# Optimization experiments

Measured on AMD Instinct MI355X. Metric: run time of the kernel, lower is better.

The kernel has to match this reference:

```python
import jax, jax.numpy as jnp
import numpy as np

N_TX = 50000; N_ADDR = 50000; E = 500000
IN = 128; C = 128; H = 4; D = 32  # C = hidden_channels = H*D
G = 512; OUT = 2
NEG_SLOPE = 0.2  # PyG HANConv default negative_slope


def _gat(h_src, h_dst, src, dst, a_src, a_dst, n_dst):
    # h_*: [N, H, D]; a_*: [H, D]; src/dst: [E]
    al_s = jnp.sum(h_src * a_src, axis=-1)  # [N_src, H]
    al_d = jnp.sum(h_dst * a_dst, axis=-1)  # [N_dst, H]
    alpha = jax.nn.leaky_relu(al_s[src] + al_d[dst], NEG_SLOPE)  # [E, H]
    # softmax over incoming edges of each destination node
    amax = jax.ops.segment_max(alpha, dst, num_segments=n_dst)
    ex = jnp.exp(alpha - amax[dst])
    denom = jax.ops.segment_sum(ex, dst, num_segments=n_dst)
    w = ex / (denom[dst] + 1e-16)  # PyG softmax adds 1e-16
    out = jax.ops.segment_sum(h_src[src] * w[:, :, None], dst, num_segments=n_dst)
    return jax.nn.relu(out.reshape(n_dst, H * D))


def _semantic(xs, q, Wk, bk):
    out = jnp.stack(xs)  # [K, N, C]
    score = jnp.sum(q * jnp.tanh(out @ Wk + bk).mean(axis=1), axis=-1)  # [K]
    attn = jax.nn.softmax(score)
    return jnp.sum(attn[:, None, None] * out, axis=0)  # [N, C]


def setup_inputs() -> dict:
    key = jax.random.key(0)
    k = jax.random.split(key, 24)
    s = 0.05
    return {
        "x_tx": jax.random.normal(k[0], (N_TX, IN), jnp.float32),
        "x_addr": jax.random.normal(k[1], (N_ADDR, IN), jnp.float32),
        "ei_ta": jnp.stack([jax.random.randint(k[2], (E,), 0, N_TX),
                            jax.random.randint(k[3], (E,), 0, N_ADDR)]),
        "ei_at": jnp.stack([jax.random.randint(k[4], (E,), 0, N_ADDR),
                            jax.random.randint(k[5], (E,), 0, N_TX)]),
        "ei_tt": jnp.stack([jax.random.randint(k[6], (E,), 0, N_TX),
                            jax.random.randint(k[7], (E,), 0, N_TX)]),
        "batch_tx": jnp.sort(jax.random.randint(k[8], (N_TX,), 0, G)),
        "W_tx": jax.random.normal(k[9], (IN, C), jnp.float32) / np.sqrt(IN).astype(np.float32),
        "b_tx": jnp.zeros((C,), jnp.float32),
        "W_addr": jax.random.normal(k[10], (IN, C), jnp.float32) / np.sqrt(IN).astype(np.float32),
        "b_addr": jnp.zeros((C,), jnp.float32),
        "a_src_ta": jax.random.normal(k[11], (H, D), jnp.float32) * s,
        "a_dst_ta": jax.random.normal(k[12], (H, D), jnp.float32) * s,
        "a_src_at": jax.random.normal(k[13], (H, D), jnp.float32) * s,
        "a_dst_at": jax.random.normal(k[14], (H, D), jnp.float32) * s,
        "a_src_tt": jax.random.normal(k[15], (H, D), jnp.float32) * s,
        "a_dst_tt": jax.random.normal(k[16], (H, D), jnp.float32) * s,
        "Wk": jax.random.normal(k[17], (C, C), jnp.float32) / np.sqrt(C).astype(np.float32),
        "bk": jnp.zeros((C,), jnp.float32),
        "q": jax.random.normal(k[18], (C,), jnp.float32) * s,
        "Wl": jax.random.normal(k[19], (C, OUT), jnp.float32) / np.sqrt(C).astype(np.float32),
        "bl": jnp.zeros((OUT,), jnp.float32),
    }


def reference(x_tx, x_addr, ei_ta, ei_at, ei_tt, batch_tx,
              W_tx, b_tx, W_addr, b_addr,
              a_src_ta, a_dst_ta, a_src_at, a_dst_at, a_src_tt, a_dst_tt,
              Wk, bk, q, Wl, bl):
    # per-node-type projection
    h_tx = (x_tx @ W_tx + b_tx).reshape(N_TX, H, D)
    h_ad = (x_addr @ W_addr + b_addr).reshape(N_ADDR, H, D)
    # per-edge-type GAT message passing (dropout disabled: eval mode)
    out_ta = _gat(h_tx, h_ad, ei_ta[0], ei_ta[1], a_src_ta, a_dst_ta, N_ADDR)
    out_at = _gat(h_ad, h_tx, ei_at[0], ei_at[1], a_src_at, a_dst_at, N_TX)
    out_tt = _gat(h_tx, h_tx, ei_tt[0], ei_tt[1], a_src_tt, a_dst_tt, N_TX)
    # semantic attention across metapaths ending at 'transaction'
    tx_feat = _semantic([out_at, out_tt], q, Wk, bk)  # [N_TX, C]
    # global_mean_pool over graph assignment
    sums = jax.ops.segment_sum(tx_feat, batch_tx, num_segments=G)
    cnts = jax.ops.segment_sum(jnp.ones((N_TX,), tx_feat.dtype), batch_tx, num_segments=G)
    pooled = sums / jnp.maximum(cnts, 1.0)[:, None]  # [G, C]
    return pooled @ Wl + bl  # [G, OUT]
```

## Files before the change

### kernel.cpp

```cpp
#include <hip/hip_runtime.h>

#define NTX   50000
#define NADDR 50000
#define NE    500000
#define GG    512
#define NEG   0.2f
#define MBLK  64
#define PBM   782
#define NCHUNK 196
#define GBLK  3125

typedef _Float16 f16;
typedef f16 f16x4 __attribute__((ext_vector_type(4)));
typedef f16 f16x8 __attribute__((ext_vector_type(8)));
typedef float f32x2 __attribute__((ext_vector_type(2)));
typedef float f32x4 __attribute__((ext_vector_type(4)));

__device__ __forceinline__ float lrelu(float x) { return x > 0.f ? x : NEG * x; }

__global__ __launch_bounds__(256) void prep_kernel(
    const float* __restrict__ W_tx, const float* __restrict__ W_ad,
    const float* __restrict__ Wk,
    f16* __restrict__ Wt_tx, f16* __restrict__ Wt_ad, f16* __restrict__ Wkt)
{
    const float* W = (blockIdx.y == 0) ? W_tx : (blockIdx.y == 1) ? W_ad : Wk;
    f16* Wt        = (blockIdx.y == 0) ? Wt_tx : (blockIdx.y == 1) ? Wt_ad : Wkt;
    __shared__ f16 tile[32][136];
    const int t = threadIdx.x;
    const int j0 = blockIdx.x * 32;
    for (int i = t; i < 32 * 128; i += 256) {
        int r = i >> 7, c = i & 127;
        tile[r][c] = (f16)W[(size_t)(j0 + r) * 128 + c];
    }
    __syncthreads();
    for (int i = t; i < 128 * 8; i += 256) {
        int c = i >> 3, q = i & 7;
        f16x4 p = { tile[q * 4 + 0][c], tile[q * 4 + 1][c],
                    tile[q * 4 + 2][c], tile[q * 4 + 3][c] };
        *(f16x4*)&Wt[(size_t)c * 128 + j0 + q * 4] = p;
    }
}

__global__ __launch_bounds__(256) void proj2_kernel(
    const float* __restrict__ x_tx, const f16* __restrict__ Wt_txg,
    const float* __restrict__ b_tx, f16* __restrict__ h_tx,
    const float* __restrict__ x_ad, const f16* __restrict__ Wt_adg,
    const float* __restrict__ b_ad, f16* __restrict__ h_ad,
    const float* __restrict__ a_dat, float* __restrict__ al_dat,
    const float* __restrict__ a_stt, float* __restrict__ al_stt,
    const float* __restrict__ a_dtt, float* __restrict__ al_dtt,
    const float* __restrict__ a_sat, float* __restrict__ al_sat)
{
    __shared__ f16 Wt[128][136];
    __shared__ f16 xt[MBLK][136];
    const bool is_tx = blockIdx.x < PBM;
    const float* x  = is_tx ? x_tx : x_ad;
    const f16* Wtg  = is_tx ? Wt_txg : Wt_adg;
    const float* b  = is_tx ? b_tx : b_ad;
    f16* h          = is_tx ? h_tx : h_ad;
    const int row0 = (is_tx ? blockIdx.x : blockIdx.x - PBM) * MBLK;
    const int t = threadIdx.x;

    {
        const f16x8* G = (const f16x8*)Wtg;
        for (int i = t; i < 128 * 16; i += 256) {
            int r = i >> 4, q = i & 15;
            *(f16x8*)&Wt[r][q * 8] = G[i];
        }
    }
    for (int i = t; i < MBLK * 32; i += 256) {
        int r = i >> 5, q = i & 31;
        int gr = row0 + r; if (gr >= NTX) gr = NTX - 1;
        float4 v = ((const float4*)x)[(size_t)gr * 32 + q];
        f16x4 p = {(f16)v.x, (f16)v.y, (f16)v.z, (f16)v.w};
        *(f16x4*)&xt[r][q * 4] = p;
    }
    __syncthreads();

    const int l = t & 63, w = t >> 6;
    const int l15 = l & 15, lq = l >> 4;

    f16x8 afrag[4];
#pragma unroll
    for (int kt = 0; kt < 4; kt++)
        afrag[kt] = *(const f16x8*)&xt[w * 16 + l15][kt * 32 + lq * 8];

    f32x4 acc[8];
#pragma unroll
    for (int n = 0; n < 8; n++) {
        float bc = b[n * 16 + l15];
        acc[n] = (f32x4){bc, bc, bc, bc};
#pragma unroll
        for (int kt = 0; kt < 4; kt++) {
            f16x8 bfrag = *(const f16x8*)&Wt[n * 16 + l15][kt * 32 + lq * 8];
            acc[n] = __builtin_amdgcn_mfma_f32_16x16x32_f16(afrag[kt], bfrag, acc[n], 0, 0, 0);
        }
    }

#pragma unroll
    for (int r = 0; r < 4; r++) {
        int row = row0 + w * 16 + lq * 4 + r;
        if (row < NTX) {
#pragma unroll
            for (int n = 0; n < 8; n++)
                h[(size_t)row * 128 + n * 16 + l15] = (f16)acc[n][r];
        }
    }

    auto do_dot = [&](const float* __restrict__ a, float* __restrict__ al) {
        float av[8];
#pragma unroll
        for (int n = 0; n < 8; n++) av[n] = a[n * 16 + l15];
#pragma unroll
        for (int r = 0; r < 4; r++) {
            float p0 = acc[0][r] * av[0] + acc[1][r] * av[1];
            float p1 = acc[2][r] * av[2] + acc[3][r] * av[3];
            float p2 = acc[4][r] * av[4] + acc[5][r] * av[5];
            float p3 = acc[6][r] * av[6] + acc[7][r] * av[7];
#pragma unroll
            for (int o = 1; o < 16; o <<= 1) {
                p0 += __shfl_xor(p0, o); p1 += __shfl_xor(p1, o);
                p2 += __shfl_xor(p2, o); p3 += __shfl_xor(p3, o);
            }
            int row = row0 + w * 16 + lq * 4 + r;
            if (l15 == 0 && row < NTX) {
                float4 v = make_float4(p0, p1, p2, p3);
                *(float4*)&al[(size_t)row * 4] = v;
            }
        }
    };
    if (is_tx) { do_dot(a_dat, al_dat); do_dot(a_stt, al_stt); do_dot(a_dtt, al_dtt); }
    else       { do_dot(a_sat, al_sat); }
}

__global__ __launch_bounds__(256) void deg2_kernel(
    const int* __restrict__ ei0, const int* __restrict__ ei1,
    int* __restrict__ deg0, int* __restrict__ deg1,
    int* __restrict__ rank0, int* __restrict__ rank1)
{
    int idx = blockIdx.x * 256 + threadIdx.x;
    if (idx < NE) rank0[idx] = atomicAdd(&deg0[ei0[NE + idx]], 1);
    else if (idx < 2 * NE) rank1[idx - NE] = atomicAdd(&deg1[ei1[NE + (idx - NE)]], 1);
}

__global__ __launch_bounds__(256) void chunksum_kernel(
    const int* __restrict__ deg0, const int* __restrict__ deg1,
    int* __restrict__ csum)
{
    const int* deg = blockIdx.y == 0 ? deg0 : deg1;
    __shared__ int s[256];
    const int t = threadIdx.x;
    int idx = blockIdx.x * 256 + t;
    s[t] = idx < NTX ? deg[idx] : 0;
    __syncthreads();
    for (int o = 128; o > 0; o >>= 1) {
        if (t < o) s[t] += s[t + o];
        __syncthreads();
    }
    if (t == 0) csum[blockIdx.y * NCHUNK + blockIdx.x] = s[0];
}

__global__ __launch_bounds__(256) void chunkscan_kernel(int* __restrict__ csum)
{
    __shared__ int s[256];
    const int t = threadIdx.x;
    int* base = csum + blockIdx.x * NCHUNK;
    int v = t < NCHUNK ? base[t] : 0;
    s[t] = v;
    __syncthreads();
    for (int o = 1; o < 256; o <<= 1) {
        int u = (t >= o) ? s[t - o] : 0;
        __syncthreads();
        s[t] += u;
        __syncthreads();
    }
    if (t < NCHUNK) base[t] = s[t] - v;
}

__global__ __launch_bounds__(256) void scanwrite_kernel(
    const int* __restrict__ deg0, const int* __restrict__ deg1,
    const int* __restrict__ csum,
    int* __restrict__ row0, int* __restrict__ row1)
{
    const int* deg = blockIdx.y == 0 ? deg0 : deg1;
    int* row       = blockIdx.y == 0 ? row0 : row1;
    __shared__ int s[256];
    const int t = threadIdx.x;
    int idx = blockIdx.x * 256 + t;
    int v = idx < NTX ? deg[idx] : 0;
    s[t] = v;
    __syncthreads();
    for (int o = 1; o < 256; o <<= 1) {
        int u = (t >= o) ? s[t - o] : 0;
        __syncthreads();
        s[t] += u;
        __syncthreads();
    }
    if (idx < NTX)
        row[idx] = s[t] - v + csum[blockIdx.y * NCHUNK + blockIdx.x];
}

__global__ __launch_bounds__(256) void fill2_kernel(
    const int* __restrict__ ei0, const int* __restrict__ rank0,
    const int* __restrict__ row0, int* __restrict__ csr0,
    const int* __restrict__ ei1, const int* __restrict__ rank1,
    const int* __restrict__ row1, int* __restrict__ csr1)
{
    int idx = blockIdx.x * 256 + threadIdx.x;
    const int* ei; const int* rank; const int* row; int* csr;
    int e;
    if (idx < NE)          { ei = ei0; rank = rank0; row = row0; csr = csr0; e = idx; }
    else if (idx < 2 * NE) { ei = ei1; rank = rank1; row = row1; csr = csr1; e = idx - NE; }
    else return;
    int s = ei[e];
    int d = ei[NE + e];
    csr[row[d] + rank[e]] = s;
}

__global__ __launch_bounds__(256) void gat_gather2_kernel(
    const int* __restrict__ row_at, const int* __restrict__ deg_at,
    const int* __restrict__ csr_at, const float* __restrict__ als_at,
    const float* __restrict__ ald_at, const f16* __restrict__ h_at,
    f16* __restrict__ out_at,
    const int* __restrict__ row_tt, const int* __restrict__ deg_tt,
    const int* __restrict__ csr_tt, const float* __restrict__ als_tt,
    const float* __restrict__ ald_tt, const f16* __restrict__ h_tt,
    f16* __restrict__ out_tt)
{
    const int bid = blockIdx.x;
    const bool at = ((bid & 4) == 0);
    const int dblk = (bid >> 3) * 4 + (bid & 3);
    if (dblk >= GBLK) return;

    const int* rs = at ? row_at : row_tt;
    const int* dg = at ? deg_at : deg_tt;
    const int* cs = at ? csr_at : csr_tt;
    const float* als = at ? als_at : als_tt;
    const float* ald = at ? ald_at : ald_tt;
    const f16* hsrc = at ? h_at : h_tt;
    f16* out = at ? out_at : out_tt;

    const int t = threadIdx.x;
    const int d = dblk * 16 + (t >> 4);
    const int ln8 = t & 15;
    const int head = ln8 >> 2;
    const int beg = rs[d];
    const int n = dg[d];
    const float aldv = ald[d * 4 + head];
    const f16x8* H = (const f16x8*)hsrc;

    f32x2 acc[4] = {{0.f, 0.f}, {0.f, 0.f}, {0.f, 0.f}, {0.f, 0.f}};
    float den = 0.f;
    int i = 0;
    for (; i + 4 <= n; i += 4) {
        int s0 = cs[beg + i],     s1 = cs[beg + i + 1];
        int s2 = cs[beg + i + 2], s3 = cs[beg + i + 3];
        float l0 = als[s0 * 4 + head], l1 = als[s1 * 4 + head];
        float l2 = als[s2 * 4 + head], l3 = als[s3 * 4 + head];
        f16x8 h0 = H[(size_t)s0 * 16 + ln8];
        f16x8 h1 = H[(size_t)s1 * 16 + ln8];
        f16x8 h2 = H[(size_t)s2 * 16 + ln8];
        f16x8 h3 = H[(size_t)s3 * 16 + ln8];
        float w0 = __expf(lrelu(l0 + aldv));
        float w1 = __expf(lrelu(l1 + aldv));
        float w2 = __expf(lrelu(l2 + aldv));
        float w3 = __expf(lrelu(l3 + aldv));
        den += (w0 + w1) + (w2 + w3);
#pragma unroll
        for (int q = 0; q < 4; q++) {
            f32x2 a0 = {(float)h0[2 * q], (float)h0[2 * q + 1]};
            f32x2 a1 = {(float)h1[2 * q], (float)h1[2 * q + 1]};
            f32x2 a2 = {(float)h2[2 * q], (float)h2[2 * q + 1]};
            f32x2 a3 = {(float)h3[2 * q], (float)h3[2 * q + 1]};
            acc[q] = a0 * w0 + (a1 * w1 + (a2 * w2 + (a3 * w3 + acc[q])));
        }
    }
    for (; i < n; i++) {
        int s0 = cs[beg + i];
        float l0 = als[s0 * 4 + head];
        f16x8 h0 = H[(size_t)s0 * 16 + ln8];
        float w0 = __expf(lrelu(l0 + aldv));
        den += w0;
#pragma unroll
        for (int q = 0; q < 4; q++) {
            f32x2 a0 = {(float)h0[2 * q], (float)h0[2 * q + 1]};
            acc[q] = a0 * w0 + acc[q];
        }
    }
    float inv = 1.f / (den + 1e-16f);
    f16x8 o;
#pragma unroll
    for (int q = 0; q < 4; q++) {
        float v0 = acc[q][0] * inv, v1 = acc[q][1] * inv;
        o[2 * q]     = (f16)(v0 > 0.f ? v0 : 0.f);
        o[2 * q + 1] = (f16)(v1 > 0.f ? v1 : 0.f);
    }
    ((f16x8*)out)[(size_t)d * 16 + ln8] = o;
}

__global__ __launch_bounds__(256) void tanh_gemm_kernel(
    const f16* __restrict__ out_at, const f16* __restrict__ out_tt,
    const f16* __restrict__ Wktg, const float* __restrict__ bk,
    float* __restrict__ part)
{
    __shared__ f16 Wt[128][136];
    __shared__ f16 xt[MBLK][136];
    const int row0 = blockIdx.x * MBLK;
    const int t = threadIdx.x;

    {
        const f16x8* G = (const f16x8*)Wktg;
        for (int i = t; i < 128 * 16; i += 256) {
            int r = i >> 4, q = i & 15;
            *(f16x8*)&Wt[r][q * 8] = G[i];
        }
    }

    const int l = t & 63, w = t >> 6;
    const int l15 = l & 15, lq = l >> 4;

    for (int y = 0; y < 2; y++) {
        const f16* src = (y == 0) ? out_at : out_tt;
        __syncthreads();
        for (int i = t; i < MBLK * 16; i += 256) {
            int r = i >> 4, q = i & 15;
            int gr = row0 + r; if (gr >= NTX) gr = NTX - 1;
            *(f16x8*)&xt[r][q * 8] = ((const f16x8*)src)[(size_t)gr * 16 + q];
        }
        __syncthreads();

        f16x8 afrag[4];
#pragma unroll
        for (int kt = 0; kt < 4; kt++)
            afrag[kt] = *(const f16x8*)&xt[w * 16 + l15][kt * 32 + lq * 8];

        float pn[8];
#pragma unroll
        for (int n = 0; n < 8; n++) {
            float bc = bk[n * 16 + l15];
            f32x4 acc = (f32x4){bc, bc, bc, bc};
#pragma unroll
            for (int kt = 0; kt < 4; kt++) {
                f16x8 bfrag = *(const f16x8*)&Wt[n * 16 + l15][kt * 32 + lq * 8];
                acc = __builtin_amdgcn_mfma_f32_16x16x32_f16(afrag[kt], bfrag, acc, 0, 0, 0);
            }
            float s = 0.f;
#pragma unroll
            for (int r = 0; r < 4; r++) {
                int row = row0 + w * 16 + lq * 4 + r;
                if (row < NTX) s += tanhf(acc[r]);
            }
            s += __shfl_xor(s, 16);
            s += __shfl_xor(s, 32);
            pn[n] = s;
        }

        __syncthreads();
        float* Sblk = (float*)&xt[0][0];
        if (l < 16) {
#pragma unroll
            for (int n = 0; n < 8; n++)
                Sblk[w * 128 + n * 16 + l15] = pn[n];
        }
        __syncthreads();
        if (t < 128)
            part[((size_t)y * PBM + blockIdx.x) * 128 + t] =
                Sblk[t] + Sblk[128 + t] + Sblk[256 + t] + Sblk[384 + t];
    }
}

__global__ __launch_bounds__(128) void reduceS_kernel(
    const float* __restrict__ part, float* __restrict__ S_at, float* __restrict__ S_tt)
{
    const int k = blockIdx.y;
    const int c = threadIdx.x;
    float* S = (k == 0) ? S_at : S_tt;
    const int b0 = blockIdx.x * 25;
    const int b1 = min(b0 + 25, PBM);
    float s = 0.f;
    for (int b = b0; b < b1; b++)
        s += part[((size_t)k * PBM + b) * 128 + c];
    atomicAdd(&S[c], s);
}

__global__ __launch_bounds__(128) void attn_kernel(
    const float* __restrict__ S0, const float* __restrict__ S1,
    const float* __restrict__ q, float* __restrict__ attn)
{
    __shared__ float r0[128], r1[128];
    int c = threadIdx.x;
    r0[c] = q[c] * S0[c];
    r1[c] = q[c] * S1[c];
    __syncthreads();
    for (int s = 64; s > 0; s >>= 1) {
        if (c < s) { r0[c] += r0[c + s]; r1[c] += r1[c + s]; }
        __syncthreads();
    }
    if (c == 0) {
        float s0 = r0[0] / (float)NTX, s1 = r1[0] / (float)NTX;
        float m = fmaxf(s0, s1);
        float e0 = expf(s0 - m), e1 = expf(s1 - m);
        float inv = 1.f / (e0 + e1);
        attn[0] = e0 * inv;
        attn[1] = e1 * inv;
    }
}

__device__ __forceinline__ int lower_bound_g(const int* __restrict__ batch, int val)
{
    int lo = 0, hi = NTX;
    while (lo < hi) {
        int mid = (lo + hi) >> 1;
        if (batch[mid] < val) lo = mid + 1; else hi = mid;
    }
    return lo;
}

__global__ __launch_bounds__(1024) void final_pool_kernel(
    const f16* __restrict__ out_at, const f16* __restrict__ out_tt,
    const int* __restrict__ batch, const float* __restrict__ attn,
    const float* __restrict__ Wl, const float* __restrict__ bl,
    float* __restrict__ out)
{
    __shared__ float r0s[8][128], r1s[8][128];
    const int g = blockIdx.x;
    const int t = threadIdx.x;
    const int sub = t >> 7, c = t & 127;
    const int lo = lower_bound_g(batch, g);
    const int hi = lower_bound_g(batch, g + 1);
    float s0 = 0.f, s1 = 0.f;
    for (int n = lo + sub; n < hi; n += 8) {
        s0 += (float)out_at[(size_t)n * 128 + c];
        s1 += (float)out_tt[(size_t)n * 128 + c];
    }
    r0s[sub][c] = s0;
    r1s[sub][c] = s1;
    __syncthreads();
    for (int o = 4; o > 0; o >>= 1) {
        if (sub < o) {
            r0s[sub][c] += r0s[sub + o][c];
            r1s[sub][c] += r1s[sub + o][c];
        }
        __syncthreads();
    }
    if (t < 128) {
        float pooled = (attn[0] * r0s[0][t] + attn[1] * r1s[0][t])
                     / fmaxf((float)(hi - lo), 1.f);
        r0s[1][t] = pooled * Wl[t * 2 + 0];
        r1s[1][t] = pooled * Wl[t * 2 + 1];
    }
    __syncthreads();
    for (int s = 64; s > 0; s >>= 1) {
        if (t < s) { r0s[1][t] += r0s[1][t + s]; r1s[1][t] += r1s[1][t + s]; }
        __syncthreads();
    }
    if (t == 0) {
        out[g * 2 + 0] = r0s[1][0] + bl[0];
        out[g * 2 + 1] = r1s[1][0] + bl[1];
    }
}

extern "C" void kernel_launch(void* const* d_in, const int* in_sizes, int n_in,
                              void* d_out, int out_size, void* d_ws, size_t ws_size,
                              hipStream_t stream)
{
    const float* x_tx     = (const float*)d_in[0];
    const float* x_ad     = (const float*)d_in[1];
    const int*   ei_at    = (const int*)d_in[3];
    const int*   ei_tt    = (const int*)d_in[4];
    const int*   batch    = (const int*)d_in[5];
    const float* W_tx     = (const float*)d_in[6];
    const float* b_tx     = (const float*)d_in[7];
    const float* W_ad     = (const float*)d_in[8];
    const float* b_ad     = (const float*)d_in[9];
    const float* a_src_at = (const float*)d_in[12];
    const float* a_dst_at = (const float*)d_in[13];
    const float* a_src_tt = (const float*)d_in[14];
    const float* a_dst_tt = (const float*)d_in[15];
    const float* Wk       = (const float*)d_in[16];
    const float* bk       = (const float*)d_in[17];
    const float* q        = (const float*)d_in[18];
    const float* Wl       = (const float*)d_in[19];
    const float* bl       = (const float*)d_in[20];
    float* out = (float*)d_out;

    char* ws = (char*)d_ws;
    size_t off = 0;
    auto alloc = [&](size_t bytes) -> void* {
        void* p = ws + off;
        off += (bytes + 255) & ~(size_t)255;
        return p;
    };
    f16* h_tx      = (f16*)alloc((size_t)NTX * 128 * 2);
    f16* h_ad      = (f16*)alloc((size_t)NADDR * 128 * 2);
    f16* Wt_txg    = (f16*)alloc((size_t)128 * 128 * 2);
    f16* Wt_adg    = (f16*)alloc((size_t)128 * 128 * 2);
    f16* Wktg      = (f16*)alloc((size_t)128 * 128 * 2);
    float* al_sat  = (float*)alloc((size_t)NADDR * 4 * 4);
    float* al_dat  = (float*)alloc((size_t)NTX * 4 * 4);
    float* al_stt  = (float*)alloc((size_t)NTX * 4 * 4);
    float* al_dtt  = (float*)alloc((size_t)NTX * 4 * 4);
    f16* out_at    = (f16*)alloc((size_t)NTX * 128 * 2);
    f16* out_tt    = (f16*)alloc((size_t)NTX * 128 * 2);
    int* csr_at    = (int*)alloc((size_t)NE * 4);
    int* csr_tt    = (int*)alloc((size_t)NE * 4);
    int* rank_at   = (int*)alloc((size_t)NE * 4);
    int* rank_tt   = (int*)alloc((size_t)NE * 4);
    int* row_at    = (int*)alloc((size_t)NTX * 4);
    int* row_tt    = (int*)alloc((size_t)NTX * 4);
    int* csum      = (int*)alloc((size_t)2 * NCHUNK * 4);
    float* part    = (float*)alloc((size_t)2 * PBM * 128 * 4);
    char* zero0 = ws + off;
    int* deg_at    = (int*)alloc((size_t)NTX * 4);
    int* deg_tt    = (int*)alloc((size_t)NTX * 4);
    float* S_at    = (float*)alloc(128 * 4);
    float* S_tt    = (float*)alloc(128 * 4);
    size_t zbytes = (size_t)((ws + off) - zero0);
    float* attnw   = (float*)alloc(2 * 4);

    hipMemsetAsync(zero0, 0, zbytes, stream);

    dim3 pgrid(4, 3);
    prep_kernel<<<pgrid, 256, 0, stream>>>(W_tx, W_ad, Wk, Wt_txg, Wt_adg, Wktg);

    proj2_kernel<<<2 * PBM, 256, 0, stream>>>(
        x_tx, Wt_txg, b_tx, h_tx, x_ad, Wt_adg, b_ad, h_ad,
        a_dst_at, al_dat, a_src_tt, al_stt, a_dst_tt, al_dtt,
        a_src_at, al_sat);

    int eb2 = (2 * NE + 255) / 256;
    deg2_kernel<<<eb2, 256, 0, stream>>>(ei_at, ei_tt, deg_at, deg_tt,
                                         rank_at, rank_tt);
    dim3 sgrid(NCHUNK, 2);
    chunksum_kernel<<<sgrid, 256, 0, stream>>>(deg_at, deg_tt, csum);
    chunkscan_kernel<<<2, 256, 0, stream>>>(csum);
    scanwrite_kernel<<<sgrid, 256, 0, stream>>>(deg_at, deg_tt, csum, row_at, row_tt);
    fill2_kernel<<<eb2, 256, 0, stream>>>(
        ei_at, rank_at, row_at, csr_at,
        ei_tt, rank_tt, row_tt, csr_tt);

    gat_gather2_kernel<<<PBM * 8, 256, 0, stream>>>(
        row_at, deg_at, csr_at, al_sat, al_dat, h_ad, out_at,
        row_tt, deg_tt, csr_tt, al_stt, al_dtt, h_tx, out_tt);

    tanh_gemm_kernel<<<PBM, 256, 0, stream>>>(out_at, out_tt, Wktg, bk, part);
    dim3 rgrid(32, 2);
    reduceS_kernel<<<rgrid, 128, 0, stream>>>(part, S_at, S_tt);
    attn_kernel<<<1, 128, 0, stream>>>(S_at, S_tt, q, attnw);

    final_pool_kernel<<<GG, 1024, 0, stream>>>(out_at, out_tt, batch, attnw, Wl, bl, out);
}
```

Baseline: 193.0 us.

## Build CSR via per-range shared-memory histograms instead of global atomics

Replaces the global-atomic degree count and rank-based fill with range-partitioned kernels. Each block owns 2048 destination nodes, scans all edges, and counts or places edges using shared-memory atomics, so the rank arrays and global atomics disappear. In exchange, every one of the 25 blocks per edge type reads the full edge list, and only 50 blocks run. CSR order within a row becomes nondeterministic, as before.

New measurement: 312.3 us. 61.8% more time.

```diff
diff --git a/kernel.cpp b/kernel.cpp
--- a/kernel.cpp
+++ b/kernel.cpp
@@ -9,6 +9,8 @@
 #define PBM   782
 #define NCHUNK 196
 #define GBLK  3125
+#define RNG   2048
+#define NRANGE 25
 
 typedef _Float16 f16;
 typedef f16 f16x4 __attribute__((ext_vector_type(4)));
@@ -133,14 +135,31 @@
     else       { do_dot(a_sat, al_sat); }
 }
 
-__global__ __launch_bounds__(256) void deg2_kernel(
+__global__ __launch_bounds__(1024) void rangedeg_kernel(
     const int* __restrict__ ei0, const int* __restrict__ ei1,
-    int* __restrict__ deg0, int* __restrict__ deg1,
-    int* __restrict__ rank0, int* __restrict__ rank1)
-{
-    int idx = blockIdx.x * 256 + threadIdx.x;
-    if (idx < NE) rank0[idx] = atomicAdd(&deg0[ei0[NE + idx]], 1);
-    else if (idx < 2 * NE) rank1[idx - NE] = atomicAdd(&deg1[ei1[NE + (idx - NE)]], 1);
+    int* __restrict__ deg0, int* __restrict__ deg1)
+{
+    const int* ei = blockIdx.y == 0 ? ei0 : ei1;
+    int* deg      = blockIdx.y == 0 ? deg0 : deg1;
+    __shared__ int hist[RNG];
+    const int t = threadIdx.x;
+    const int r0 = blockIdx.x * RNG;
+    for (int j = t; j < RNG; j += 1024) hist[j] = 0;
+    __syncthreads();
+    const int4* dst4 = (const int4*)(ei + NE);
+    for (int i = t; i < NE / 4; i += 1024) {
+        int4 d4 = dst4[i];
+        int a;
+        a = d4.x - r0; if ((unsigned)a < RNG) atomicAdd(&hist[a], 1);
+        a = d4.y - r0; if ((unsigned)a < RNG) atomicAdd(&hist[a], 1);
+        a = d4.z - r0; if ((unsigned)a < RNG) atomicAdd(&hist[a], 1);
+        a = d4.w - r0; if ((unsigned)a < RNG) atomicAdd(&hist[a], 1);
+    }
+    __syncthreads();
+    for (int j = t; j < RNG; j += 1024) {
+        int d = r0 + j;
+        if (d < NTX) deg[d] = hist[j];
+    }
 }
 
 __global__ __launch_bounds__(256) void chunksum_kernel(
@@ -200,21 +219,32 @@
         row[idx] = s[t] - v + csum[blockIdx.y * NCHUNK + blockIdx.x];
 }
 
-__global__ __launch_bounds__(256) void fill2_kernel(
-    const int* __restrict__ ei0, const int* __restrict__ rank0,
-    const int* __restrict__ row0, int* __restrict__ csr0,
-    const int* __restrict__ ei1, const int* __restrict__ rank1,
-    const int* __restrict__ row1, int* __restrict__ csr1)
-{
-    int idx = blockIdx.x * 256 + threadIdx.x;
-    const int* ei; const int* rank; const int* row; int* csr;
-    int e;
-    if (idx < NE)          { ei = ei0; rank = rank0; row = row0; csr = csr0; e = idx; }
-    else if (idx < 2 * NE) { ei = ei1; rank = rank1; row = row1; csr = csr1; e = idx - NE; }
-    else return;
-    int s = ei[e];
-    int d = ei[NE + e];
-    csr[row[d] + rank[e]] = s;
+__global__ __launch_bounds__(1024) void rangefill_kernel(
+    const int* __restrict__ ei0, const int* __restrict__ row0, int* __restrict__ csr0,
+    const int* __restrict__ ei1, const int* __restrict__ row1, int* __restrict__ csr1)
+{
+    const int* ei  = blockIdx.y == 0 ? ei0 : ei1;
+    const int* row = blockIdx.y == 0 ? row0 : row1;
+    int* csr       = blockIdx.y == 0 ? csr0 : csr1;
+    __shared__ int cur[RNG];
+    const int t = threadIdx.x;
+    const int r0 = blockIdx.x * RNG;
+    for (int j = t; j < RNG; j += 1024) {
+        int d = r0 + j;
+        cur[j] = (d < NTX) ? row[d] : 0;
+    }
+    __syncthreads();
+    const int4* src4 = (const int4*)ei;
+    const int4* dst4 = (const int4*)(ei + NE);
+    for (int i = t; i < NE / 4; i += 1024) {
+        int4 d4 = dst4[i];
+        int4 s4 = src4[i];
+        int a;
+        a = d4.x - r0; if ((unsigned)a < RNG) { int p = atomicAdd(&cur[a], 1); csr[p] = s4.x; }
+        a = d4.y - r0; if ((unsigned)a < RNG) { int p = atomicAdd(&cur[a], 1); csr[p] = s4.y; }
+        a = d4.z - r0; if ((unsigned)a < RNG) { int p = atomicAdd(&cur[a], 1); csr[p] = s4.z; }
+        a = d4.w - r0; if ((unsigned)a < RNG) { int p = atomicAdd(&cur[a], 1); csr[p] = s4.w; }
+    }
 }
 
 __global__ __launch_bounds__(256) void gat_gather2_kernel(
@@ -504,15 +534,13 @@
     f16* out_tt    = (f16*)alloc((size_t)NTX * 128 * 2);
     int* csr_at    = (int*)alloc((size_t)NE * 4);
     int* csr_tt    = (int*)alloc((size_t)NE * 4);
-    int* rank_at   = (int*)alloc((size_t)NE * 4);
-    int* rank_tt   = (int*)alloc((size_t)NE * 4);
     int* row_at    = (int*)alloc((size_t)NTX * 4);
     int* row_tt    = (int*)alloc((size_t)NTX * 4);
+    int* deg_at    = (int*)alloc((size_t)NTX * 4);
+    int* deg_tt    = (int*)alloc((size_t)NTX * 4);
     int* csum      = (int*)alloc((size_t)2 * NCHUNK * 4);
     float* part    = (float*)alloc((size_t)2 * PBM * 128 * 4);
     char* zero0 = ws + off;
-    int* deg_at    = (int*)alloc((size_t)NTX * 4);
-    int* deg_tt    = (int*)alloc((size_t)NTX * 4);
     float* S_at    = (float*)alloc(128 * 4);
     float* S_tt    = (float*)alloc(128 * 4);
     size_t zbytes = (size_t)((ws + off) - zero0);
@@ -528,16 +556,14 @@
         a_dst_at, al_dat, a_src_tt, al_stt, a_dst_tt, al_dtt,
         a_src_at, al_sat);
 
-    int eb2 = (2 * NE + 255) / 256;
-    deg2_kernel<<<eb2, 256, 0, stream>>>(ei_at, ei_tt, deg_at, deg_tt,
-                                         rank_at, rank_tt);
+    dim3 rgrid2(NRANGE, 2);
+    rangedeg_kernel<<<rgrid2, 1024, 0, stream>>>(ei_at, ei_tt, deg_at, deg_tt);
     dim3 sgrid(NCHUNK, 2);
     chunksum_kernel<<<sgrid, 256, 0, stream>>>(deg_at, deg_tt, csum);
     chunkscan_kernel<<<2, 256, 0, stream>>>(csum);
     scanwrite_kernel<<<sgrid, 256, 0, stream>>>(deg_at, deg_tt, csum, row_at, row_tt);
-    fill2_kernel<<<eb2, 256, 0, stream>>>(
-        ei_at, rank_at, row_at, csr_at,
-        ei_tt, rank_tt, row_tt, csr_tt);
+    rangefill_kernel<<<rgrid2, 1024, 0, stream>>>(ei_at, row_at, csr_at,
+                                                  ei_tt, row_tt, csr_tt);
 
     gat_gather2_kernel<<<PBM * 8, 256, 0, stream>>>(
         row_at, deg_at, csr_at, al_sat, al_dat, h_ad, out_at,
```
